# Kernel optimization log

Measured on AMD Instinct MI355X. Metric: run time of the kernel, lower is better.

## Reference

```python
import jax, jax.numpy as jnp
import numpy as np

EMBED_DIM = 768
FF_MULT = 4
HIDDEN = EMBED_DIM * FF_MULT
BATCH, SEQ = 32, 1024
EPS = 1e-6


def rmsnorm(x, g):
    # RMSNorm over last dim with learned scale g
    return x * jax.lax.rsqrt(jnp.mean(x * x, axis=-1, keepdims=True) + EPS) * g


def act_quant(x):
    # per-token int8 absmax quantization (BitNet b1.58)
    scale = 127.0 / jnp.clip(jnp.max(jnp.abs(x), axis=-1, keepdims=True), 1e-5, None)
    return jnp.clip(jnp.round(x * scale), -128.0, 127.0) / scale


def weight_quant(w):
    # per-tensor ternary (1.58-bit) absmean quantization
    scale = 1.0 / jnp.clip(jnp.mean(jnp.abs(w)), 1e-5, None)
    return jnp.clip(jnp.round(w * scale), -1.0, 1.0) / scale


def bitlinear(x, w, g):
    xn = rmsnorm(x, g)
    # straight-through estimator: forward uses quantized values
    xq = xn + jax.lax.stop_gradient(act_quant(xn) - xn)
    wq = w + jax.lax.stop_gradient(weight_quant(w) - w)
    return jnp.einsum('bsd,fd->bsf', xq, wq)


def setup_inputs() -> dict:
    key = jax.random.key(0)
    k1, k2, k3 = jax.random.split(key, 3)
    x = jax.random.normal(k1, (BATCH, SEQ, EMBED_DIM), dtype=jnp.float32)
    w1 = jax.random.normal(k2, (HIDDEN, EMBED_DIM), dtype=jnp.float32) * 0.02
    w2 = jax.random.normal(k3, (EMBED_DIM, HIDDEN), dtype=jnp.float32) * 0.02
    g1 = jnp.ones((EMBED_DIM,), dtype=jnp.float32)
    g2 = jnp.ones((HIDDEN,), dtype=jnp.float32)
    return {"x": x, "w1": w1, "g1": g1, "w2": w2, "g2": g2}


def reference(x, w1, g1, w2, g2):
    # BitFeedForward: BitLinear -> GELU (exact, matches nn.GELU) -> BitLinear
    # Dropout(p=0.0) is identity.
    h = jax.nn.gelu(bitlinear(x, w1, g1), approximate=False)
    return bitlinear(h, w2, g2)
```

## Files before the change

kernel.cpp:

```cpp
#include <hip/hip_runtime.h>
#include <hip/hip_bf16.h>
#include <hip/hip_fp16.h>
#include <math.h>

#define TOKENS 32768
#define EMBED  768
#define HIDDEN 3072
#define WELEMS (EMBED*HIDDEN)

typedef __attribute__((ext_vector_type(4))) int i32x4;
typedef __attribute__((ext_vector_type(4))) signed char i8x4;
typedef signed char i8;

__device__ __forceinline__ float wave_reduce_sum(float v) {
    for (int o = 32; o > 0; o >>= 1) v += __shfl_down(v, o);
    return v;
}
__device__ __forceinline__ float wave_reduce_max(float v) {
    for (int o = 32; o > 0; o >>= 1) v = fmaxf(v, __shfl_down(v, o));
    return v;
}

__global__ __launch_bounds__(256) void k_abs_partial(const float* __restrict__ w,
                                                     float* __restrict__ out, int n) {
    float s = 0.f;
    for (int i = blockIdx.x * 256 + threadIdx.x; i < n; i += gridDim.x * 256)
        s += fabsf(w[i]);
    __shared__ float red[4];
    s = wave_reduce_sum(s);
    if ((threadIdx.x & 63) == 0) red[threadIdx.x >> 6] = s;
    __syncthreads();
    if (threadIdx.x == 0) out[blockIdx.x] = red[0] + red[1] + red[2] + red[3];
}

__global__ __launch_bounds__(256) void k_finalize(const float* __restrict__ p,
                                                  float* __restrict__ m) {
    __shared__ float r1[4], r2[4];
    float s1 = 0.f, s2 = 0.f;
    for (int i = threadIdx.x; i < 512; i += 256) { s1 += p[i]; s2 += p[512 + i]; }
    s1 = wave_reduce_sum(s1); s2 = wave_reduce_sum(s2);
    if ((threadIdx.x & 63) == 0) { r1[threadIdx.x >> 6] = s1; r2[threadIdx.x >> 6] = s2; }
    __syncthreads();
    if (threadIdx.x == 0) {
        float m1 = (r1[0] + r1[1] + r1[2] + r1[3]) / (float)WELEMS;
        float m2 = (r2[0] + r2[1] + r2[2] + r2[3]) / (float)WELEMS;
        m[0] = fmaxf(m1, 1e-5f);
        m[1] = fmaxf(m2, 1e-5f);
    }
}

__global__ __launch_bounds__(256) void k_quant_w(const float* __restrict__ w,
                                                 i8* __restrict__ wq,
                                                 const float* __restrict__ mp, int n) {
    const float inv = 1.0f / mp[0];
    for (int i = blockIdx.x * 256 + threadIdx.x; i < n; i += gridDim.x * 256) {
        float q = rintf(w[i] * inv);
        q = fminf(1.f, fmaxf(-1.f, q));
        wq[i] = (i8)(int)q;
    }
}

template <int D>
__global__ __launch_bounds__(256) void k_rms_quant_f32(const float* __restrict__ x,
                                                       const float* __restrict__ g,
                                                       i8* __restrict__ xq,
                                                       float* __restrict__ sc) {
    constexpr int NV = D / 4;
    constexpr int IT = (NV + 255) / 256;
    __shared__ float reds[4], redm[4];
    const int t = blockIdx.x;
    const float4* xp = reinterpret_cast<const float4*>(x + (size_t)t * D);
    const float4* gp = reinterpret_cast<const float4*>(g);
    float4 xg[IT];
    float ssq = 0.f, amax = 0.f;
#pragma unroll
    for (int i = 0; i < IT; ++i) {
        const int idx = i * 256 + (int)threadIdx.x;
        const bool act = (NV % 256 == 0) || (idx < NV);
        if (act) {
            float4 v = xp[idx];
            float4 gv = gp[idx];
            ssq += v.x * v.x + v.y * v.y + v.z * v.z + v.w * v.w;
            xg[i].x = v.x * gv.x; xg[i].y = v.y * gv.y;
            xg[i].z = v.z * gv.z; xg[i].w = v.w * gv.w;
            amax = fmaxf(amax, fmaxf(fmaxf(fabsf(xg[i].x), fabsf(xg[i].y)),
                                     fmaxf(fabsf(xg[i].z), fabsf(xg[i].w))));
        } else {
            xg[i].x = xg[i].y = xg[i].z = xg[i].w = 0.f;
        }
    }
    ssq = wave_reduce_sum(ssq);
    amax = wave_reduce_max(amax);
    if ((threadIdx.x & 63) == 0) { reds[threadIdx.x >> 6] = ssq; redm[threadIdx.x >> 6] = amax; }
    __syncthreads();
    const float S = reds[0] + reds[1] + reds[2] + reds[3];
    const float A = fmaxf(fmaxf(redm[0], redm[1]), fmaxf(redm[2], redm[3]));
    const float rs = (float)(1.0 / sqrt((double)S / D + 1e-6));
    const float an = fmaxf(A * rs, 1e-5f);
    const float qs = rs * (127.0f / an);
    if (threadIdx.x == 0) sc[t] = an * (1.0f / 127.0f);
    i8x4* op = reinterpret_cast<i8x4*>(xq + (size_t)t * D);
#pragma unroll
    for (int i = 0; i < IT; ++i) {
        const int idx = i * 256 + (int)threadIdx.x;
        const bool act = (NV % 256 == 0) || (idx < NV);
        if (act) {
            i8x4 r;
            r[0] = (i8)(int)fminf(127.f, fmaxf(-128.f, rintf(xg[i].x * qs)));
            r[1] = (i8)(int)fminf(127.f, fmaxf(-128.f, rintf(xg[i].y * qs)));
            r[2] = (i8)(int)fminf(127.f, fmaxf(-128.f, rintf(xg[i].z * qs)));
            r[3] = (i8)(int)fminf(127.f, fmaxf(-128.f, rintf(xg[i].w * qs)));
            op[idx] = r;
        }
    }
}

template <int D>
__global__ __launch_bounds__(256) void k_rms_quant_f16(const __half* __restrict__ x,
                                                       const float* __restrict__ g,
                                                       i8* __restrict__ xq,
                                                       float* __restrict__ sc) {
    constexpr int NV = D / 8;
    constexpr int IT = (NV + 255) / 256;
    __shared__ float reds[4], redm[4];
    const int t = blockIdx.x;
    const int4* xp = reinterpret_cast<const int4*>(x + (size_t)t * D);
    const float4* gp = reinterpret_cast<const float4*>(g);
    float xg[IT][8];
    float ssq = 0.f, amax = 0.f;
#pragma unroll
    for (int i = 0; i < IT; ++i) {
        const int idx = i * 256 + (int)threadIdx.x;
        const bool act = (NV % 256 == 0) || (idx < NV);
        if (act) {
            int4 raw = xp[idx];
            const __half2* hp = reinterpret_cast<const __half2*>(&raw);
            float4 g0 = gp[idx * 2];
            float4 g1 = gp[idx * 2 + 1];
            float gv[8] = {g0.x, g0.y, g0.z, g0.w, g1.x, g1.y, g1.z, g1.w};
#pragma unroll
            for (int j = 0; j < 4; ++j) {
                float2 f = __half22float2(hp[j]);
                float a0 = f.x, a1 = f.y;
                ssq += a0 * a0 + a1 * a1;
                xg[i][j * 2]     = a0 * gv[j * 2];
                xg[i][j * 2 + 1] = a1 * gv[j * 2 + 1];
                amax = fmaxf(amax, fmaxf(fabsf(xg[i][j * 2]), fabsf(xg[i][j * 2 + 1])));
            }
        } else {
#pragma unroll
            for (int j = 0; j < 8; ++j) xg[i][j] = 0.f;
        }
    }
    ssq = wave_reduce_sum(ssq);
    amax = wave_reduce_max(amax);
    if ((threadIdx.x & 63) == 0) { reds[threadIdx.x >> 6] = ssq; redm[threadIdx.x >> 6] = amax; }
    __syncthreads();
    const float S = reds[0] + reds[1] + reds[2] + reds[3];
    const float A = fmaxf(fmaxf(redm[0], redm[1]), fmaxf(redm[2], redm[3]));
    const float rs = (float)(1.0 / sqrt((double)S / D + 1e-6));
    const float an = fmaxf(A * rs, 1e-5f);
    const float qs = rs * (127.0f / an);
    if (threadIdx.x == 0) sc[t] = an * (1.0f / 127.0f);
    i8x4* op = reinterpret_cast<i8x4*>(xq + (size_t)t * D);
#pragma unroll
    for (int i = 0; i < IT; ++i) {
        const int idx = i * 256 + (int)threadIdx.x;
        const bool act = (NV % 256 == 0) || (idx < NV);
        if (act) {
            i8x4 r0, r1;
#pragma unroll
            for (int j = 0; j < 4; ++j)
                r0[j] = (i8)(int)fminf(127.f, fmaxf(-128.f, rintf(xg[i][j] * qs)));
#pragma unroll
            for (int j = 0; j < 4; ++j)
                r1[j] = (i8)(int)fminf(127.f, fmaxf(-128.f, rintf(xg[i][4 + j] * qs)));
            op[idx * 2]     = r0;
            op[idx * 2 + 1] = r1;
        }
    }
}

template <bool GELU, typename OutT>
__global__ __launch_bounds__(256, 4) void k_gemm_i8(const i8* __restrict__ A,
                                                    const i8* __restrict__ B,
                                                    OutT* __restrict__ C,
                                                    const float* __restrict__ rsc,
                                                    const float* __restrict__ msc,
                                                    int N, int K) {
    __shared__ i8 As[128 * 128];
    __shared__ i8 Bs[128 * 128];
    const int tid  = threadIdx.x;
    const int lane = tid & 63;
    const int wave = tid >> 6;
    const int wr = wave >> 1, wc = wave & 1;
    const size_t rowBase = (size_t)blockIdx.y * 128;
    const size_t colBase = (size_t)blockIdx.x * 128;
    const float ms = msc[0];

    i32x4 acc[4][4] = {};

    const int srow = tid >> 3;
    const int cc   = tid & 7;
    const int gcol = (cc ^ (srow & 7)) * 16;
    const i8* gA0 = A + (rowBase + srow) * (size_t)K + gcol;
    const i8* gB0 = B + (colBase + srow) * (size_t)K + gcol;
    const int lOff = srow * 128 + cc * 16;

    const int frow = lane & 15;
    const int fko  = (lane >> 4) * 16;
    const int rswz = (frow & 7) << 4;

    for (int k0 = 0; k0 < K; k0 += 128) {
#pragma unroll
        for (int r = 0; r < 4; ++r) {
            __builtin_amdgcn_global_load_lds(
                (const __attribute__((address_space(1))) void*)(gA0 + (size_t)r * 32 * K + k0),
                (__attribute__((address_space(3))) void*)(&As[lOff + r * 32 * 128]), 16, 0, 0);
            __builtin_amdgcn_global_load_lds(
                (const __attribute__((address_space(1))) void*)(gB0 + (size_t)r * 32 * K + k0),
                (__attribute__((address_space(3))) void*)(&Bs[lOff + r * 32 * 128]), 16, 0, 0);
        }
        __syncthreads();
#pragma unroll
        for (int ks = 0; ks < 2; ++ks) {
            i32x4 af[4], bv[4];
#pragma unroll
            for (int mi = 0; mi < 4; ++mi)
                af[mi] = *(const i32x4*)(&As[(wr * 64 + mi * 16 + frow) * 128
                                             + ((ks * 64 + fko) ^ rswz)]);
#pragma unroll
            for (int ni = 0; ni < 4; ++ni)
                bv[ni] = *(const i32x4*)(&Bs[(wc * 64 + ni * 16 + frow) * 128
                                             + ((ks * 64 + fko) ^ rswz)]);
#pragma unroll
            for (int mi = 0; mi < 4; ++mi)
#pragma unroll
                for (int ni = 0; ni < 4; ++ni)
                    acc[mi][ni] = __builtin_amdgcn_mfma_i32_16x16x64_i8(
                        af[mi], bv[ni], acc[mi][ni], 0, 0, 0);
        }
        __syncthreads();
    }

    const int ccol = lane & 15;
    const int crg  = lane >> 4;
#pragma unroll
    for (int mi = 0; mi < 4; ++mi) {
#pragma unroll
        for (int i = 0; i < 4; ++i) {
            size_t row = rowBase + wr * 64 + mi * 16 + crg * 4 + i;
            float rscale = rsc[row] * ms;
#pragma unroll
            for (int ni = 0; ni < 4; ++ni) {
                size_t col = colBase + wc * 64 + ni * 16 + ccol;
                float v = (float)acc[mi][ni][i] * rscale;
                if (GELU) v = 0.5f * v * (1.0f + erff(v * 0.70710678118654752440f));
                C[row * (size_t)N + col] = (OutT)v;
            }
        }
    }
}

extern "C" void kernel_launch(void* const* d_in, const int* in_sizes, int n_in,
                              void* d_out, int out_size, void* d_ws, size_t ws_size,
                              hipStream_t stream) {
    const float* x  = (const float*)d_in[0];
    const float* w1 = (const float*)d_in[1];
    const float* g1 = (const float*)d_in[2];
    const float* w2 = (const float*)d_in[3];
    const float* g2 = (const float*)d_in[4];
    float* out = (float*)d_out;

    char* ws = (char*)d_ws;
    float* partials = (float*)ws;
    float* mvals    = (float*)(ws + 4096);
    float* a        = (float*)(ws + 4352);
    float* b        = (float*)(ws + 135424);
    i8*    wq1      = (i8*)(ws + 266496);
    i8*    wq2      = (i8*)(ws + 2625792);
    const size_t FIXED = 4985088;
    char* chunkMem = ws + FIXED;

    const size_t PER_TOK = 768 + 6144 + 3072;
    size_t avail = (ws_size > FIXED) ? (ws_size - FIXED) : 0;
    long long ch = (long long)(avail / PER_TOK);
    ch &= ~127LL;
    if (ch < 128) ch = 128;
    if (ch > TOKENS) ch = TOKENS;
    const int CH = (int)ch;

    k_abs_partial<<<512, 256, 0, stream>>>(w1, partials, WELEMS);
    k_abs_partial<<<512, 256, 0, stream>>>(w2, partials + 512, WELEMS);
    k_finalize<<<1, 256, 0, stream>>>(partials, mvals);
    k_quant_w<<<2048, 256, 0, stream>>>(w1, wq1, mvals + 0, WELEMS);
    k_quant_w<<<2048, 256, 0, stream>>>(w2, wq2, mvals + 1, WELEMS);

    for (int base = 0; base < TOKENS; base += CH) {
        const int rows = (TOKENS - base < CH) ? (TOKENS - base) : CH;
        i8*     xqc = (i8*)chunkMem;
        __half* hc  = (__half*)(chunkMem + (size_t)CH * 768);
        i8*     hqc = (i8*)(chunkMem + (size_t)CH * 768 + (size_t)CH * 6144);

        k_rms_quant_f32<EMBED><<<rows, 256, 0, stream>>>(
            x + (size_t)base * EMBED, g1, xqc, a + base);
        k_gemm_i8<true, __half><<<dim3(HIDDEN / 128, rows / 128), 256, 0, stream>>>(
            xqc, wq1, hc, a + base, mvals + 0, HIDDEN, EMBED);
        k_rms_quant_f16<HIDDEN><<<rows, 256, 0, stream>>>(
            hc, g2, hqc, b + base);
        k_gemm_i8<false, float><<<dim3(EMBED / 128, rows / 128), 256, 0, stream>>>(
            hqc, wq2, out + (size_t)base * EMBED, b + base, mvals + 1, EMBED, HIDDEN);
    }
}
```

Measured before the change: 360.8 us.

## Widen int8 GEMM tile to 128x256 with XCD block swizzle and fast GELU

The int8 GEMM now uses 512-thread blocks computing 128x256 output tiles, doubling the B tile in shared memory to raise operand reuse per A load. A 1D grid is remapped so consecutive tiles land on the same XCD for better L2 locality. The exact erff GELU is replaced with a polynomial erf approximation using a hardware reciprocal and fast exp, cutting epilogue cost at a small accuracy cost. Larger LDS footprint may reduce occupancy.

```diff
diff --git a/kernel.cpp b/kernel.cpp
--- a/kernel.cpp
+++ b/kernel.cpp
@@ -19,6 +19,20 @@
 __device__ __forceinline__ float wave_reduce_max(float v) {
     for (int o = 32; o > 0; o >>= 1) v = fmaxf(v, __shfl_down(v, o));
     return v;
+}
+
+__device__ __forceinline__ float gelu_fast(float v) {
+    const float z  = fabsf(v) * 0.70710678118654752440f;
+    const float t  = __builtin_amdgcn_rcpf(fmaf(0.3275911f, z, 1.0f));
+    float p = fmaf(1.061405429f, t, -1.453152027f);
+    p = fmaf(p, t, 1.421413741f);
+    p = fmaf(p, t, -0.284496736f);
+    p = fmaf(p, t, 0.254829592f);
+    p = p * t;
+    const float e   = __expf(-z * z);
+    const float erf = fmaf(-p, e, 1.0f);
+    const float se  = (v >= 0.f) ? erf : -erf;
+    return 0.5f * v * (1.0f + se);
 }
 
 __global__ __launch_bounds__(256) void k_abs_partial(const float* __restrict__ w,
@@ -182,20 +196,28 @@
 }
 
 template <bool GELU, typename OutT>
-__global__ __launch_bounds__(256, 4) void k_gemm_i8(const i8* __restrict__ A,
+__global__ __launch_bounds__(512, 4) void k_gemm_i8(const i8* __restrict__ A,
                                                     const i8* __restrict__ B,
                                                     OutT* __restrict__ C,
                                                     const float* __restrict__ rsc,
                                                     const float* __restrict__ msc,
-                                                    int N, int K) {
+                                                    int nbx, int N, int K) {
     __shared__ i8 As[128 * 128];
-    __shared__ i8 Bs[128 * 128];
+    __shared__ i8 Bs[256 * 128];
+    const int nwg = (int)gridDim.x;
+    const int id  = (int)blockIdx.x;
+    const int q = nwg >> 3, r = nwg & 7;
+    const int xcd = id & 7, sub = id >> 3;
+    const int swz = (xcd < r ? xcd * (q + 1) : r * (q + 1) + (xcd - r) * q) + sub;
+    const int bx = swz % nbx;
+    const int by = swz / nbx;
+
     const int tid  = threadIdx.x;
     const int lane = tid & 63;
     const int wave = tid >> 6;
-    const int wr = wave >> 1, wc = wave & 1;
-    const size_t rowBase = (size_t)blockIdx.y * 128;
-    const size_t colBase = (size_t)blockIdx.x * 128;
+    const int wr = wave >> 2, wc = wave & 3;
+    const size_t rowBase = (size_t)by * 128;
+    const size_t colBase = (size_t)bx * 256;
     const float ms = msc[0];
 
     i32x4 acc[4][4] = {};
@@ -213,14 +235,15 @@
 
     for (int k0 = 0; k0 < K; k0 += 128) {
 #pragma unroll
-        for (int r = 0; r < 4; ++r) {
+        for (int r2 = 0; r2 < 2; ++r2)
             __builtin_amdgcn_global_load_lds(
-                (const __attribute__((address_space(1))) void*)(gA0 + (size_t)r * 32 * K + k0),
-                (__attribute__((address_space(3))) void*)(&As[lOff + r * 32 * 128]), 16, 0, 0);
+                (const __attribute__((address_space(1))) void*)(gA0 + (size_t)r2 * 64 * K + k0),
+                (__attribute__((address_space(3))) void*)(&As[lOff + r2 * 64 * 128]), 16, 0, 0);
+#pragma unroll
+        for (int r4 = 0; r4 < 4; ++r4)
             __builtin_amdgcn_global_load_lds(
-                (const __attribute__((address_space(1))) void*)(gB0 + (size_t)r * 32 * K + k0),
-                (__attribute__((address_space(3))) void*)(&Bs[lOff + r * 32 * 128]), 16, 0, 0);
-        }
+                (const __attribute__((address_space(1))) void*)(gB0 + (size_t)r4 * 64 * K + k0),
+                (__attribute__((address_space(3))) void*)(&Bs[lOff + r4 * 64 * 128]), 16, 0, 0);
         __syncthreads();
 #pragma unroll
         for (int ks = 0; ks < 2; ++ks) {
@@ -255,7 +278,7 @@
             for (int ni = 0; ni < 4; ++ni) {
                 size_t col = colBase + wc * 64 + ni * 16 + ccol;
                 float v = (float)acc[mi][ni][i] * rscale;
-                if (GELU) v = 0.5f * v * (1.0f + erff(v * 0.70710678118654752440f));
+                if (GELU) v = gelu_fast(v);
                 C[row * (size_t)N + col] = (OutT)v;
             }
         }
@@ -285,8 +308,8 @@
     const size_t PER_TOK = 768 + 6144 + 3072;
     size_t avail = (ws_size > FIXED) ? (ws_size - FIXED) : 0;
     long long ch = (long long)(avail / PER_TOK);
-    ch &= ~127LL;
-    if (ch < 128) ch = 128;
+    ch &= ~255LL;
+    if (ch < 256) ch = 256;
     if (ch > TOKENS) ch = TOKENS;
     const int CH = (int)ch;
 
@@ -302,13 +325,17 @@
         __half* hc  = (__half*)(chunkMem + (size_t)CH * 768);
         i8*     hqc = (i8*)(chunkMem + (size_t)CH * 768 + (size_t)CH * 6144);
 
+        const int nby = rows / 128;
+        const int nbx1 = HIDDEN / 256;
+        const int nbx2 = EMBED / 256;
+
         k_rms_quant_f32<EMBED><<<rows, 256, 0, stream>>>(
             x + (size_t)base * EMBED, g1, xqc, a + base);
-        k_gemm_i8<true, __half><<<dim3(HIDDEN / 128, rows / 128), 256, 0, stream>>>(
-            xqc, wq1, hc, a + base, mvals + 0, HIDDEN, EMBED);
+        k_gemm_i8<true, __half><<<nbx1 * nby, 512, 0, stream>>>(
+            xqc, wq1, hc, a + base, mvals + 0, nbx1, HIDDEN, EMBED);
         k_rms_quant_f16<HIDDEN><<<rows, 256, 0, stream>>>(
             hc, g2, hqc, b + base);
-        k_gemm_i8<false, float><<<dim3(EMBED / 128, rows / 128), 256, 0, stream>>>(
-            hqc, wq2, out + (size_t)base * EMBED, b + base, mvals + 1, EMBED, HIDDEN);
-    }
-}
+        k_gemm_i8<false, float><<<nbx2 * nby, 512, 0, stream>>>(
+            hqc, wq2, out + (size_t)base * EMBED, b + base, mvals + 1, nbx2, EMBED, HIDDEN);
+    }
+}
```

New measurement: 365.2 us. About the same (+1.2%).
